# Kernel optimization log

Hardware: AMD Instinct MI355X
Metric: run time of the kernel (lower is better)

Reference implementation:

```python
import jax, jax.numpy as jnp
import numpy as np


def setup_inputs() -> dict:
    key = jax.random.key(0)
    k1, k2, k3, k4 = jax.random.split(key, 4)
    B, S, H = 1, 2048, 3072
    E, I = 4, 8192  # num_experts, intermediate_size
    x = jax.random.normal(k1, (B, S, H), dtype=jnp.float32)
    gate_w = jax.random.normal(k2, (E, H), dtype=jnp.float32) * 0.02
    w_gate_up = jax.random.normal(k3, (E, 2 * I, H), dtype=jnp.float32) * 0.02
    w_down = jax.random.normal(k4, (E, H, I), dtype=jnp.float32) * 0.02
    return {"x": x, "gate_w": gate_w, "w_gate_up": w_gate_up, "w_down": w_down, "top_k": 2}


def reference(x, gate_w, w_gate_up, w_down, top_k):
    # x: [B, S, H]; gate_w: [E, H]; w_gate_up: [E, 2I, H]; w_down: [E, H, I]
    B, S, H = x.shape
    E = gate_w.shape[0]
    # Gating: softmax over experts, then top-k values/indices
    logits = jnp.einsum('bsh,eh->bse', x, gate_w)
    probs = jax.nn.softmax(logits, axis=-1)
    gate_values, gate_indices = jax.lax.top_k(probs, top_k)  # [B, S, k]
    # Dense all-expert SwiGLU MLP (as in the original module)
    xf = x.reshape(-1, H)                                     # [N, H]
    up_states = jnp.einsum('nh,eih->nei', xf, w_gate_up)      # [N, E, 2I]
    gate, up = jnp.split(up_states, 2, axis=-1)               # [N, E, I] each
    hidden = up * jax.nn.silu(gate)                           # SwiGLU
    expert_out = jnp.einsum('nei,ehi->neh', hidden, w_down)   # [N, E, H]
    expert_out = expert_out.reshape(B, S, E, H)
    # Gather selected experts and combine with gate values
    sel = jnp.take_along_axis(expert_out, gate_indices[..., None], axis=2)  # [B, S, k, H]
    moe_output = jnp.sum(sel * gate_values[..., None], axis=2)              # [B, S, H]
    return moe_output
```

## Files before the change

kernel.cpp:

```cpp
#include <hip/hip_runtime.h>

#define S 2048
#define Hd 3072
#define NE 4
#define Id 8192
#define BM 128
#define BK 64
#define RMAX 4608

typedef __attribute__((ext_vector_type(8))) short short8;
typedef __attribute__((ext_vector_type(4))) float f32x4;

__device__ __forceinline__ unsigned short f2bf(float f) {
    unsigned u = __builtin_bit_cast(unsigned, f);
    u += 0x7FFFu + ((u >> 16) & 1u);
    return (unsigned short)(u >> 16);
}

__device__ __forceinline__ void gload_lds16(const void* g, void* l) {
    __builtin_amdgcn_global_load_lds(
        (const __attribute__((address_space(1))) unsigned int*)g,
        (__attribute__((address_space(3))) unsigned int*)l,
        16, 0, 0);
}

__global__ void gate_topk_kernel(const float* __restrict__ x,
                                 const float* __restrict__ gw,
                                 int* __restrict__ tok_e,
                                 float* __restrict__ tok_v) {
    const int t = blockIdx.x;
    const int lane = threadIdx.x & 63;
    const int wave = threadIdx.x >> 6;
    __shared__ float logits[NE];
    const float* xp = x + (size_t)t * Hd;
    const float* wp = gw + (size_t)wave * Hd;
    float s = 0.f;
    for (int h = lane; h < Hd; h += 64) s += xp[h] * wp[h];
#pragma unroll
    for (int o = 32; o > 0; o >>= 1) s += __shfl_xor(s, o);
    if (lane == 0) logits[wave] = s;
    __syncthreads();
    if (threadIdx.x == 0) {
        float m = logits[0];
#pragma unroll
        for (int e = 1; e < NE; e++) m = fmaxf(m, logits[e]);
        float p[NE]; float sum = 0.f;
#pragma unroll
        for (int e = 0; e < NE; e++) { p[e] = expf(logits[e] - m); sum += p[e]; }
        float inv = 1.f / sum;
#pragma unroll
        for (int e = 0; e < NE; e++) p[e] *= inv;
        int e0 = 0; float v0 = p[0];
#pragma unroll
        for (int e = 1; e < NE; e++) if (p[e] > v0) { e0 = e; v0 = p[e]; }
        int e1 = -1; float v1 = -1.f;
#pragma unroll
        for (int e = 0; e < NE; e++) if (e != e0 && p[e] > v1) { e1 = e; v1 = p[e]; }
        tok_e[t * 2] = e0; tok_e[t * 2 + 1] = e1;
        tok_v[t * 2] = v0; tok_v[t * 2 + 1] = v1;
    }
}

__global__ void route_kernel(const int* __restrict__ tok_e, const float* __restrict__ tok_v,
                             int* __restrict__ row_token, float* __restrict__ row_gate,
                             int* __restrict__ offsets) {
    __shared__ int cnt[NE], cur[NE], offs[NE + 1];
    const int tid = threadIdx.x;
    if (tid < NE) { cnt[tid] = 0; cur[tid] = 0; }
    __syncthreads();
    for (int i = tid; i < S * 2; i += 256) atomicAdd(&cnt[tok_e[i]], 1);
    __syncthreads();
    if (tid == 0) {
        int o = 0;
        for (int e = 0; e < NE; e++) { offs[e] = o; o += (cnt[e] + BM - 1) / BM * BM; }
        offs[NE] = o;
        for (int e = 0; e <= NE; e++) offsets[e] = offs[e];
    }
    __syncthreads();
    for (int r = tid; r < RMAX; r += 256) { row_token[r] = 0; row_gate[r] = 0.f; }
    __syncthreads();
    for (int i = tid; i < S * 2; i += 256) {
        int e = tok_e[i];
        int pos = atomicAdd(&cur[e], 1);
        int r = offs[e] + pos;
        row_token[r] = i >> 1;
        row_gate[r] = tok_v[i];
    }
}

__global__ void cvt_bf16_kernel(const float* __restrict__ src,
                                unsigned short* __restrict__ dst, size_t n8) {
    size_t stride = (size_t)gridDim.x * blockDim.x;
    for (size_t i = (size_t)blockIdx.x * blockDim.x + threadIdx.x; i < n8; i += stride) {
        size_t b = i * 8;
        f32x4 a = *(const f32x4*)(src + b);
        f32x4 c = *(const f32x4*)(src + b + 4);
        union { unsigned short u[8]; short8 v; } o;
#pragma unroll
        for (int j = 0; j < 4; j++) { o.u[j] = f2bf(a[j]); o.u[4 + j] = f2bf(c[j]); }
        *(short8*)(dst + b) = o.v;
    }
}


__global__ __launch_bounds__(256, 2)
void gemm1_bf16_kernel(const unsigned short* __restrict__ xb,
                       const unsigned short* __restrict__ wgu_b,
                       const int* __restrict__ row_token,
                       const int* __restrict__ offsets,
                       unsigned short* __restrict__ hidden) {
    __shared__ unsigned short As[BM][BK];
    __shared__ unsigned short Bg[BM][BK];
    __shared__ unsigned short Bu[BM][BK];

    const int rt = blockIdx.x, ct = blockIdx.y;
    const int rbase = rt * BM;
    const int off4 = offsets[4];
    if (rbase >= off4) return;
    int e = 3;
    if (rbase < offsets[1]) e = 0;
    else if (rbase < offsets[2]) e = 1;
    else if (rbase < offsets[3]) e = 2;

    const int tid = threadIdx.x;
    const int lane = tid & 63;
    const int wave = tid >> 6;
    const int wm = wave >> 1, wn = wave & 1;

    const unsigned short* asrc[4];
    const unsigned short* gsrc[4];
    const unsigned short* usrc[4];
#pragma unroll
    for (int i2 = 0; i2 < 4; i2++) {
        int sgi = i2 * 4 + wave;
        int row = sgi * 8 + (lane >> 3);
        int g = (lane & 7) ^ (row & 7);
        int tok = row_token[rbase + row];
        asrc[i2] = xb + (size_t)tok * Hd + g * 8;
        size_t growg = (size_t)e * (2 * Id) + (size_t)ct * 128 + row;
        gsrc[i2] = wgu_b + growg * Hd + g * 8;
        usrc[i2] = wgu_b + (growg + (size_t)Id) * Hd + g * 8;
    }

    f32x4 accg[4][4], accu[4][4];
#pragma unroll
    for (int m = 0; m < 4; m++)
#pragma unroll
        for (int n = 0; n < 4; n++) { accg[m][n] = (f32x4)0.f; accu[m][n] = (f32x4)0.f; }

    for (int k0 = 0; k0 < Hd; k0 += BK) {
        __syncthreads();
#pragma unroll
        for (int i2 = 0; i2 < 4; i2++) {
            int sgi = i2 * 4 + wave;
            gload_lds16(asrc[i2] + k0, &As[sgi * 8][0]);
            gload_lds16(gsrc[i2] + k0, &Bg[sgi * 8][0]);
            gload_lds16(usrc[i2] + k0, &Bu[sgi * 8][0]);
        }
        __syncthreads();
#pragma unroll
        for (int kk = 0; kk < 2; kk++) {
            short8 af[4], bgf[4], buf_[4];
#pragma unroll
            for (int m = 0; m < 4; m++) {
                int r = wm * 64 + m * 16 + (lane & 15);
                int slot = (kk * 4 + (lane >> 4)) ^ (r & 7);
                af[m] = *(const short8*)&As[r][slot * 8];
            }
#pragma unroll
            for (int n = 0; n < 4; n++) {
                int c = wn * 64 + n * 16 + (lane & 15);
                int slot = (kk * 4 + (lane >> 4)) ^ (c & 7);
                bgf[n] = *(const short8*)&Bg[c][slot * 8];
                buf_[n] = *(const short8*)&Bu[c][slot * 8];
            }
#pragma unroll
            for (int m = 0; m < 4; m++)
#pragma unroll
                for (int n = 0; n < 4; n++) {
                    accg[m][n] = __builtin_amdgcn_mfma_f32_16x16x32_bf16(af[m], bgf[n], accg[m][n], 0, 0, 0);
                    accu[m][n] = __builtin_amdgcn_mfma_f32_16x16x32_bf16(af[m], buf_[n], accu[m][n], 0, 0, 0);
                }
        }
    }
#pragma unroll
    for (int m = 0; m < 4; m++) {
#pragma unroll
        for (int n = 0; n < 4; n++) {
            int c = ct * 128 + wn * 64 + n * 16 + (lane & 15);
#pragma unroll
            for (int q = 0; q < 4; q++) {
                int r = rbase + wm * 64 + m * 16 + (lane >> 4) * 4 + q;
                float g = accg[m][n][q], u = accu[m][n][q];
                float hval = u * g / (1.f + expf(-g));
                hidden[(size_t)r * Id + c] = f2bf(hval);
            }
        }
    }
}

__global__ __launch_bounds__(256, 3)
void gemm2_bf16_kernel(const unsigned short* __restrict__ hidden,
                       const unsigned short* __restrict__ wd_b,
                       const int* __restrict__ row_token,
                       const float* __restrict__ row_gate,
                       const int* __restrict__ offsets,
                       float* __restrict__ out) {
    __shared__ unsigned short As[BM][BK];
    __shared__ unsigned short Bs[BM][BK];

    const int rt = blockIdx.x, ct = blockIdx.y;
    const int rbase = rt * BM;
    const int off4 = offsets[4];
    if (rbase >= off4) return;
    int e = 3;
    if (rbase < offsets[1]) e = 0;
    else if (rbase < offsets[2]) e = 1;
    else if (rbase < offsets[3]) e = 2;

    const int tid = threadIdx.x;
    const int lane = tid & 63;
    const int wave = tid >> 6;
    const int wm = wave >> 1, wn = wave & 1;

    const unsigned short* asrc[4];
    const unsigned short* bsrc[4];
#pragma unroll
    for (int i2 = 0; i2 < 4; i2++) {
        int sgi = i2 * 4 + wave;
        int row = sgi * 8 + (lane >> 3);
        int g = (lane & 7) ^ (row & 7);
        asrc[i2] = hidden + (size_t)(rbase + row) * Id + g * 8;
        bsrc[i2] = wd_b + ((size_t)e * Hd + (size_t)ct * 128 + row) * Id + g * 8;
    }

    f32x4 acc[4][4];
#pragma unroll
    for (int m = 0; m < 4; m++)
#pragma unroll
        for (int n = 0; n < 4; n++) acc[m][n] = (f32x4)0.f;

    for (int k0 = 0; k0 < Id; k0 += BK) {
        __syncthreads();
#pragma unroll
        for (int i2 = 0; i2 < 4; i2++) {
            int sgi = i2 * 4 + wave;
            gload_lds16(asrc[i2] + k0, &As[sgi * 8][0]);
            gload_lds16(bsrc[i2] + k0, &Bs[sgi * 8][0]);
        }
        __syncthreads();
#pragma unroll
        for (int kk = 0; kk < 2; kk++) {
            short8 af[4], bf[4];
#pragma unroll
            for (int m = 0; m < 4; m++) {
                int r = wm * 64 + m * 16 + (lane & 15);
                int slot = (kk * 4 + (lane >> 4)) ^ (r & 7);
                af[m] = *(const short8*)&As[r][slot * 8];
            }
#pragma unroll
            for (int n = 0; n < 4; n++) {
                int c = wn * 64 + n * 16 + (lane & 15);
                int slot = (kk * 4 + (lane >> 4)) ^ (c & 7);
                bf[n] = *(const short8*)&Bs[c][slot * 8];
            }
#pragma unroll
            for (int m = 0; m < 4; m++)
#pragma unroll
                for (int n = 0; n < 4; n++)
                    acc[m][n] = __builtin_amdgcn_mfma_f32_16x16x32_bf16(af[m], bf[n], acc[m][n], 0, 0, 0);
        }
    }
#pragma unroll
    for (int m = 0; m < 4; m++) {
#pragma unroll
        for (int n = 0; n < 4; n++) {
            int c = ct * 128 + wn * 64 + n * 16 + (lane & 15);
#pragma unroll
            for (int q = 0; q < 4; q++) {
                int r = rbase + wm * 64 + m * 16 + (lane >> 4) * 4 + q;
                int tok = row_token[r];
                float gv = row_gate[r];
                if (gv != 0.f)
                    atomicAdd(&out[(size_t)tok * Hd + c], gv * acc[m][n][q]);
            }
        }
    }
}


__global__ __launch_bounds__(256, 2)
void gemm1_f32_kernel(const unsigned short* __restrict__ xb,
                      const float* __restrict__ wgu,
                      const int* __restrict__ row_token,
                      const int* __restrict__ offsets,
                      unsigned short* __restrict__ hidden) {
    __shared__ unsigned short As[BM][BK];
    __shared__ unsigned short Bg[BM][BK];
    __shared__ unsigned short Bu[BM][BK];

    const int rt = blockIdx.x, ct = blockIdx.y;
    const int rbase = rt * BM;
    const int off4 = offsets[4];
    if (rbase >= off4) return;
    int e = 3;
    if (rbase < offsets[1]) e = 0;
    else if (rbase < offsets[2]) e = 1;
    else if (rbase < offsets[3]) e = 2;

    const int tid = threadIdx.x;
    const int lane = tid & 63;
    const int wave = tid >> 6;
    const int wm = wave >> 1, wn = wave & 1;

    const unsigned short* asrc[4];
#pragma unroll
    for (int i2 = 0; i2 < 4; i2++) {
        int sgi = i2 * 4 + wave;
        int row = sgi * 8 + (lane >> 3);
        int g = (lane & 7) ^ (row & 7);
        int tok = row_token[rbase + row];
        asrc[i2] = xb + (size_t)tok * Hd + g * 8;
    }
    const int col = tid >> 1;
    const int half = tid & 1;
    const size_t grow = (size_t)e * (2 * Id) + (size_t)ct * 128 + col;
    const float* bsrc_g = wgu + grow * Hd + half * 32;
    const float* bsrc_u = wgu + (grow + (size_t)Id) * Hd + half * 32;
    const int csw = col & 7;

    f32x4 accg[4][4], accu[4][4];
#pragma unroll
    for (int m = 0; m < 4; m++)
#pragma unroll
        for (int n = 0; n < 4; n++) { accg[m][n] = (f32x4)0.f; accu[m][n] = (f32x4)0.f; }

    for (int k0 = 0; k0 < Hd; k0 += BK) {
        __syncthreads();
#pragma unroll
        for (int i2 = 0; i2 < 4; i2++) {
            int sgi = i2 * 4 + wave;
            gload_lds16(asrc[i2] + k0, &As[sgi * 8][0]);
        }
        {
            const float* pg = bsrc_g + k0;
            const float* pu = bsrc_u + k0;
            f32x4 vg[8], vu[8];
#pragma unroll
            for (int j = 0; j < 8; j++) vg[j] = *(const f32x4*)(pg + j * 4);
#pragma unroll
            for (int j = 0; j < 8; j++) vu[j] = *(const f32x4*)(pu + j * 4);
#pragma unroll
            for (int j = 0; j < 4; j++) {
                union { unsigned short u[8]; short8 v8; } wg_, wu_;
#pragma unroll
                for (int q = 0; q < 4; q++) {
                    wg_.u[q] = f2bf(vg[2 * j][q]); wg_.u[4 + q] = f2bf(vg[2 * j + 1][q]);
                    wu_.u[q] = f2bf(vu[2 * j][q]); wu_.u[4 + q] = f2bf(vu[2 * j + 1][q]);
                }
                int gs = (half * 4 + j) ^ csw;
                *(short8*)&Bg[col][gs * 8] = wg_.v8;
                *(short8*)&Bu[col][gs * 8] = wu_.v8;
            }
        }
        __syncthreads();
#pragma unroll
        for (int kk = 0; kk < 2; kk++) {
            short8 af[4], bgf[4], buf_[4];
#pragma unroll
            for (int m = 0; m < 4; m++) {
                int r = wm * 64 + m * 16 + (lane & 15);
                int slot = (kk * 4 + (lane >> 4)) ^ (r & 7);
                af[m] = *(const short8*)&As[r][slot * 8];
            }
#pragma unroll
            for (int n = 0; n < 4; n++) {
                int c = wn * 64 + n * 16 + (lane & 15);
                int slot = (kk * 4 + (lane >> 4)) ^ (c & 7);
                bgf[n] = *(const short8*)&Bg[c][slot * 8];
                buf_[n] = *(const short8*)&Bu[c][slot * 8];
            }
#pragma unroll
            for (int m = 0; m < 4; m++)
#pragma unroll
                for (int n = 0; n < 4; n++) {
                    accg[m][n] = __builtin_amdgcn_mfma_f32_16x16x32_bf16(af[m], bgf[n], accg[m][n], 0, 0, 0);
                    accu[m][n] = __builtin_amdgcn_mfma_f32_16x16x32_bf16(af[m], buf_[n], accu[m][n], 0, 0, 0);
                }
        }
    }
#pragma unroll
    for (int m = 0; m < 4; m++) {
#pragma unroll
        for (int n = 0; n < 4; n++) {
            int c = ct * 128 + wn * 64 + n * 16 + (lane & 15);
#pragma unroll
            for (int q = 0; q < 4; q++) {
                int r = rbase + wm * 64 + m * 16 + (lane >> 4) * 4 + q;
                float g = accg[m][n][q], u = accu[m][n][q];
                float hval = u * g / (1.f + expf(-g));
                hidden[(size_t)r * Id + c] = f2bf(hval);
            }
        }
    }
}

__global__ __launch_bounds__(256, 2)
void gemm2_f32_kernel(const unsigned short* __restrict__ hidden,
                      const float* __restrict__ wd,
                      const int* __restrict__ row_token,
                      const float* __restrict__ row_gate,
                      const int* __restrict__ offsets,
                      float* __restrict__ out) {
    __shared__ unsigned short As[BM][BK];
    __shared__ unsigned short Bs[BM][BK];

    const int rt = blockIdx.x, ct = blockIdx.y;
    const int rbase = rt * BM;
    const int off4 = offsets[4];
    if (rbase >= off4) return;
    int e = 3;
    if (rbase < offsets[1]) e = 0;
    else if (rbase < offsets[2]) e = 1;
    else if (rbase < offsets[3]) e = 2;

    const int tid = threadIdx.x;
    const int lane = tid & 63;
    const int wave = tid >> 6;
    const int wm = wave >> 1, wn = wave & 1;

    const unsigned short* asrc[4];
#pragma unroll
    for (int i2 = 0; i2 < 4; i2++) {
        int sgi = i2 * 4 + wave;
        int row = sgi * 8 + (lane >> 3);
        int g = (lane & 7) ^ (row & 7);
        asrc[i2] = hidden + (size_t)(rbase + row) * Id + g * 8;
    }
    const int col = tid >> 1;
    const int half = tid & 1;
    const float* bsrc = wd + ((size_t)e * Hd + (size_t)ct * 128 + col) * Id + half * 32;
    const int csw = col & 7;

    f32x4 acc[4][4];
#pragma unroll
    for (int m = 0; m < 4; m++)
#pragma unroll
        for (int n = 0; n < 4; n++) acc[m][n] = (f32x4)0.f;

    for (int k0 = 0; k0 < Id; k0 += BK) {
        __syncthreads();
#pragma unroll
        for (int i2 = 0; i2 < 4; i2++) {
            int sgi = i2 * 4 + wave;
            gload_lds16(asrc[i2] + k0, &As[sgi * 8][0]);
        }
        {
            const float* pb = bsrc + k0;
            f32x4 vb[8];
#pragma unroll
            for (int j = 0; j < 8; j++) vb[j] = *(const f32x4*)(pb + j * 4);
#pragma unroll
            for (int j = 0; j < 4; j++) {
                union { unsigned short u[8]; short8 v8; } wb_;
#pragma unroll
                for (int q = 0; q < 4; q++) {
                    wb_.u[q] = f2bf(vb[2 * j][q]); wb_.u[4 + q] = f2bf(vb[2 * j + 1][q]);
                }
                int gs = (half * 4 + j) ^ csw;
                *(short8*)&Bs[col][gs * 8] = wb_.v8;
            }
        }
        __syncthreads();
#pragma unroll
        for (int kk = 0; kk < 2; kk++) {
            short8 af[4], bf[4];
#pragma unroll
            for (int m = 0; m < 4; m++) {
                int r = wm * 64 + m * 16 + (lane & 15);
                int slot = (kk * 4 + (lane >> 4)) ^ (r & 7);
                af[m] = *(const short8*)&As[r][slot * 8];
            }
#pragma unroll
            for (int n = 0; n < 4; n++) {
                int c = wn * 64 + n * 16 + (lane & 15);
                int slot = (kk * 4 + (lane >> 4)) ^ (c & 7);
                bf[n] = *(const short8*)&Bs[c][slot * 8];
            }
#pragma unroll
            for (int m = 0; m < 4; m++)
#pragma unroll
                for (int n = 0; n < 4; n++)
                    acc[m][n] = __builtin_amdgcn_mfma_f32_16x16x32_bf16(af[m], bf[n], acc[m][n], 0, 0, 0);
        }
    }
#pragma unroll
    for (int m = 0; m < 4; m++) {
#pragma unroll
        for (int n = 0; n < 4; n++) {
            int c = ct * 128 + wn * 64 + n * 16 + (lane & 15);
#pragma unroll
            for (int q = 0; q < 4; q++) {
                int r = rbase + wm * 64 + m * 16 + (lane >> 4) * 4 + q;
                int tok = row_token[r];
                float gv = row_gate[r];
                if (gv != 0.f)
                    atomicAdd(&out[(size_t)tok * Hd + c], gv * acc[m][n][q]);
            }
        }
    }
}

extern "C" void kernel_launch(void* const* d_in, const int* in_sizes, int n_in,
                              void* d_out, int out_size, void* d_ws, size_t ws_size,
                              hipStream_t stream) {
    const float* x   = (const float*)d_in[0];
    const float* gw  = (const float*)d_in[1];
    const float* wgu = (const float*)d_in[2];
    const float* wd  = (const float*)d_in[3];
    float* out = (float*)d_out;

    const size_t n_wgu = (size_t)NE * 2 * Id * Hd;
    const size_t n_wd  = (size_t)NE * Hd * Id;

    char* ws = (char*)d_ws;
    size_t o = 0;
    auto alloc = [&](size_t bytes) { void* p = ws + o; o = (o + bytes + 255) & ~(size_t)255; return p; };
    unsigned short* xb      = (unsigned short*)alloc((size_t)S * Hd * 2);
    unsigned short* hidden  = (unsigned short*)alloc((size_t)RMAX * Id * 2);
    int*   row_token = (int*)alloc(RMAX * 4);
    float* row_gate  = (float*)alloc(RMAX * 4);
    int*   offsets   = (int*)alloc(8 * 4);
    int*   tok_e     = (int*)alloc(S * 2 * 4);
    float* tok_v     = (float*)alloc(S * 2 * 4);
    size_t base_need = o;
    unsigned short* wgu_b = (unsigned short*)alloc(n_wgu * 2);
    unsigned short* wd_b  = (unsigned short*)alloc(n_wd * 2);
    const bool big = (ws_size >= o);

    hipMemsetAsync(d_out, 0, (size_t)S * Hd * 4, stream);
    gate_topk_kernel<<<S, 256, 0, stream>>>(x, gw, tok_e, tok_v);
    route_kernel<<<1, 256, 0, stream>>>(tok_e, tok_v, row_token, row_gate, offsets);
    cvt_bf16_kernel<<<1024, 256, 0, stream>>>(x, xb, (size_t)S * Hd / 8);

    if (big) {
        cvt_bf16_kernel<<<2048, 256, 0, stream>>>(wgu, wgu_b, n_wgu / 8);
        cvt_bf16_kernel<<<2048, 256, 0, stream>>>(wd, wd_b, n_wd / 8);
        gemm1_bf16_kernel<<<dim3(RMAX / BM, Id / 128), 256, 0, stream>>>(
            xb, wgu_b, row_token, offsets, hidden);
        gemm2_bf16_kernel<<<dim3(RMAX / BM, Hd / 128), 256, 0, stream>>>(
            hidden, wd_b, row_token, row_gate, offsets, out);
    } else {
        (void)base_need;
        gemm1_f32_kernel<<<dim3(RMAX / BM, Id / 128), 256, 0, stream>>>(
            xb, wgu, row_token, offsets, hidden);
        gemm2_f32_kernel<<<dim3(RMAX / BM, Hd / 128), 256, 0, stream>>>(
            hidden, wd, row_token, row_gate, offsets, out);
    }
}
```

Baseline: 1.381 ms.

## Replace bf16 expert GEMMs with 256x256 double-buffered 8-wave pipelined kernels

Rewrites both grouped expert GEMMs to use 256-row tiles with 8 waves (512 threads), double-buffered LDS, and a four-phase schedule. Each phase interleaves global-to-LDS prefetch of the next K slice with MFMA on the current one, using partial vmcnt waits, barriers and setprio. Routing padding grows to 256 rows per expert and RMAX rises to fit. The gate/up weights are interleaved in 16-row groups so one B tile holds both. The aim is to hide memory latency and raise arithmetic intensity per tile, at the cost of more padded rows, higher register pressure and 64KB of LDS per block.

```diff
diff --git a/kernel.cpp b/kernel.cpp
--- a/kernel.cpp
+++ b/kernel.cpp
@@ -4,9 +4,8 @@
 #define Hd 3072
 #define NE 4
 #define Id 8192
-#define BM 128
 #define BK 64
-#define RMAX 4608
+#define RMAX 5120
 
 typedef __attribute__((ext_vector_type(8))) short short8;
 typedef __attribute__((ext_vector_type(4))) float f32x4;
@@ -22,6 +21,12 @@
         (const __attribute__((address_space(1))) unsigned int*)g,
         (__attribute__((address_space(3))) unsigned int*)l,
         16, 0, 0);
+}
+
+__device__ __forceinline__ void phase_wait() {
+    asm volatile("s_waitcnt vmcnt(8)" ::: "memory");
+    __builtin_amdgcn_s_barrier();
+    __builtin_amdgcn_sched_barrier(0);
 }
 
 __global__ void gate_topk_kernel(const float* __restrict__ x,
@@ -72,7 +77,7 @@
     __syncthreads();
     if (tid == 0) {
         int o = 0;
-        for (int e = 0; e < NE; e++) { offs[e] = o; o += (cnt[e] + BM - 1) / BM * BM; }
+        for (int e = 0; e < NE; e++) { offs[e] = o; o += (cnt[e] + 255) / 256 * 256; }
         offs[NE] = o;
         for (int e = 0; e <= NE; e++) offsets[e] = offs[e];
     }
@@ -103,189 +108,316 @@
 }
 
 
-__global__ __launch_bounds__(256, 2)
-void gemm1_bf16_kernel(const unsigned short* __restrict__ xb,
-                       const unsigned short* __restrict__ wgu_b,
-                       const int* __restrict__ row_token,
-                       const int* __restrict__ offsets,
-                       unsigned short* __restrict__ hidden) {
-    __shared__ unsigned short As[BM][BK];
-    __shared__ unsigned short Bg[BM][BK];
-    __shared__ unsigned short Bu[BM][BK];
+__global__ __launch_bounds__(512, 2)
+void gemm1_8p_kernel(const unsigned short* __restrict__ xb,
+                     const unsigned short* __restrict__ wgu_b,
+                     const int* __restrict__ row_token,
+                     const int* __restrict__ offsets,
+                     unsigned short* __restrict__ hidden) {
+    __shared__ unsigned short Ald[2][256][BK];
+    __shared__ unsigned short Bld[2][256][BK];
 
     const int rt = blockIdx.x, ct = blockIdx.y;
-    const int rbase = rt * BM;
-    const int off4 = offsets[4];
-    if (rbase >= off4) return;
+    const int rbase = rt * 256;
+    if (rbase >= offsets[4]) return;
     int e = 3;
     if (rbase < offsets[1]) e = 0;
     else if (rbase < offsets[2]) e = 1;
     else if (rbase < offsets[3]) e = 2;
 
     const int tid = threadIdx.x;
-    const int lane = tid & 63;
-    const int wave = tid >> 6;
-    const int wm = wave >> 1, wn = wave & 1;
-
-    const unsigned short* asrc[4];
-    const unsigned short* gsrc[4];
-    const unsigned short* usrc[4];
-#pragma unroll
-    for (int i2 = 0; i2 < 4; i2++) {
-        int sgi = i2 * 4 + wave;
-        int row = sgi * 8 + (lane >> 3);
-        int g = (lane & 7) ^ (row & 7);
+    const int l = tid & 63;
+    const int w = tid >> 6;
+    const int wm = w >> 2, wn = w & 3;
+    const int lr = l >> 3;
+    const int g8 = ((l & 7) ^ lr) << 3;
+    const int c16 = l & 15, c4 = l >> 4, l7 = l & 7;
+
+    const unsigned short* aP[4]; int raD[4];
+    const unsigned short* bP[4]; int rbD[4];
+#pragma unroll
+    for (int j = 0; j < 4; j++) {
+        int r0 = w * 8 + (j & 1) * 128 + (j >> 1) * 64;
+        raD[j] = r0;
+        int row = r0 + lr;
         int tok = row_token[rbase + row];
-        asrc[i2] = xb + (size_t)tok * Hd + g * 8;
-        size_t growg = (size_t)e * (2 * Id) + (size_t)ct * 128 + row;
-        gsrc[i2] = wgu_b + growg * Hd + g * 8;
-        usrc[i2] = wgu_b + (growg + (size_t)Id) * Hd + g * 8;
-    }
-
-    f32x4 accg[4][4], accu[4][4];
-#pragma unroll
-    for (int m = 0; m < 4; m++)
-#pragma unroll
-        for (int n = 0; n < 4; n++) { accg[m][n] = (f32x4)0.f; accu[m][n] = (f32x4)0.f; }
-
-    for (int k0 = 0; k0 < Hd; k0 += BK) {
-        __syncthreads();
-#pragma unroll
-        for (int i2 = 0; i2 < 4; i2++) {
-            int sgi = i2 * 4 + wave;
-            gload_lds16(asrc[i2] + k0, &As[sgi * 8][0]);
-            gload_lds16(gsrc[i2] + k0, &Bg[sgi * 8][0]);
-            gload_lds16(usrc[i2] + k0, &Bu[sgi * 8][0]);
-        }
-        __syncthreads();
-#pragma unroll
-        for (int kk = 0; kk < 2; kk++) {
-            short8 af[4], bgf[4], buf_[4];
-#pragma unroll
-            for (int m = 0; m < 4; m++) {
-                int r = wm * 64 + m * 16 + (lane & 15);
-                int slot = (kk * 4 + (lane >> 4)) ^ (r & 7);
-                af[m] = *(const short8*)&As[r][slot * 8];
-            }
-#pragma unroll
-            for (int n = 0; n < 4; n++) {
-                int c = wn * 64 + n * 16 + (lane & 15);
-                int slot = (kk * 4 + (lane >> 4)) ^ (c & 7);
-                bgf[n] = *(const short8*)&Bg[c][slot * 8];
-                buf_[n] = *(const short8*)&Bu[c][slot * 8];
-            }
-#pragma unroll
-            for (int m = 0; m < 4; m++)
-#pragma unroll
-                for (int n = 0; n < 4; n++) {
-                    accg[m][n] = __builtin_amdgcn_mfma_f32_16x16x32_bf16(af[m], bgf[n], accg[m][n], 0, 0, 0);
-                    accu[m][n] = __builtin_amdgcn_mfma_f32_16x16x32_bf16(af[m], buf_[n], accu[m][n], 0, 0, 0);
-                }
-        }
-    }
-#pragma unroll
-    for (int m = 0; m < 4; m++) {
-#pragma unroll
-        for (int n = 0; n < 4; n++) {
-            int c = ct * 128 + wn * 64 + n * 16 + (lane & 15);
+        aP[j] = xb + (size_t)tok * Hd + g8;
+        int rb0 = (w & 3) * 8 + (w >> 2) * 64 + (j & 1) * 128 + (j >> 1) * 32;
+        rbD[j] = rb0;
+        int brow = rb0 + lr;
+        int f = brow >> 4;
+        size_t wr = (size_t)e * (2 * Id) + (size_t)(f & 1) * Id
+                  + (size_t)ct * 128 + ((f >> 1) << 4) + (brow & 15);
+        bP[j] = wgu_b + wr * Hd + g8;
+    }
+
+    f32x4 acc[8][4];
+#pragma unroll
+    for (int mi = 0; mi < 8; mi++)
+#pragma unroll
+        for (int n = 0; n < 4; n++) acc[mi][n] = (f32x4)0.f;
+
+    gload_lds16(aP[0], &Ald[0][raD[0]][0]);
+    gload_lds16(aP[1], &Ald[0][raD[1]][0]);
+    gload_lds16(bP[0], &Bld[0][rbD[0]][0]);
+    gload_lds16(bP[1], &Bld[0][rbD[1]][0]);
+    gload_lds16(aP[2], &Ald[0][raD[2]][0]);
+    gload_lds16(aP[3], &Ald[0][raD[3]][0]);
+    gload_lds16(bP[2], &Bld[0][rbD[2]][0]);
+    gload_lds16(bP[3], &Bld[0][rbD[3]][0]);
+
+    const int nt = Hd / BK;
+    for (int t = 0; t < nt; ++t) {
+        const int bufR = t & 1, bufW = bufR ^ 1;
+        const int ks = ((t + 1 < nt) ? t + 1 : nt - 1) * BK;
+        short8 afL[4][2], afH[4][2], bfL[2][2], bfH[2][2];
+        gload_lds16(aP[0] + ks, &Ald[bufW][raD[0]][0]);
+        gload_lds16(aP[1] + ks, &Ald[bufW][raD[1]][0]);
+        phase_wait();
+#pragma unroll
+        for (int mi = 0; mi < 4; mi++)
+#pragma unroll
+            for (int kk = 0; kk < 2; kk++) {
+                int row = wm * 128 + mi * 16 + c16;
+                int slot = ((kk << 2) + c4) ^ l7;
+                afL[mi][kk] = *(const short8*)&Ald[bufR][row][slot * 8];
+            }
+        gload_lds16(bP[0] + ks, &Bld[bufW][rbD[0]][0]);
+        gload_lds16(bP[1] + ks, &Bld[bufW][rbD[1]][0]);
+        phase_wait();
+#pragma unroll
+        for (int n = 0; n < 2; n++)
+#pragma unroll
+            for (int kk = 0; kk < 2; kk++) {
+                int row = wn * 64 + n * 16 + c16;
+                int slot = ((kk << 2) + c4) ^ l7;
+                bfL[n][kk] = *(const short8*)&Bld[bufR][row][slot * 8];
+            }
+        __builtin_amdgcn_s_setprio(1);
+#pragma unroll
+        for (int mi = 0; mi < 4; mi++)
+#pragma unroll
+            for (int n = 0; n < 2; n++)
+#pragma unroll
+                for (int kk = 0; kk < 2; kk++)
+                    acc[mi][n] = __builtin_amdgcn_mfma_f32_16x16x32_bf16(
+                        afL[mi][kk], bfL[n][kk], acc[mi][n], 0, 0, 0);
+        __builtin_amdgcn_s_setprio(0);
+        gload_lds16(aP[2] + ks, &Ald[bufW][raD[2]][0]);
+        gload_lds16(aP[3] + ks, &Ald[bufW][raD[3]][0]);
+        phase_wait();
+#pragma unroll
+        for (int mi = 0; mi < 4; mi++)
+#pragma unroll
+            for (int kk = 0; kk < 2; kk++) {
+                int row = wm * 128 + 64 + mi * 16 + c16;
+                int slot = ((kk << 2) + c4) ^ l7;
+                afH[mi][kk] = *(const short8*)&Ald[bufR][row][slot * 8];
+            }
+        __builtin_amdgcn_s_setprio(1);
+#pragma unroll
+        for (int mi = 0; mi < 4; mi++)
+#pragma unroll
+            for (int n = 0; n < 2; n++)
+#pragma unroll
+                for (int kk = 0; kk < 2; kk++)
+                    acc[mi + 4][n] = __builtin_amdgcn_mfma_f32_16x16x32_bf16(
+                        afH[mi][kk], bfL[n][kk], acc[mi + 4][n], 0, 0, 0);
+        __builtin_amdgcn_s_setprio(0);
+        gload_lds16(bP[2] + ks, &Bld[bufW][rbD[2]][0]);
+        gload_lds16(bP[3] + ks, &Bld[bufW][rbD[3]][0]);
+        phase_wait();
+#pragma unroll
+        for (int n = 0; n < 2; n++)
+#pragma unroll
+            for (int kk = 0; kk < 2; kk++) {
+                int row = wn * 64 + 32 + n * 16 + c16;
+                int slot = ((kk << 2) + c4) ^ l7;
+                bfH[n][kk] = *(const short8*)&Bld[bufR][row][slot * 8];
+            }
+        __builtin_amdgcn_s_setprio(1);
+#pragma unroll
+        for (int mi = 0; mi < 8; mi++)
+#pragma unroll
+            for (int n = 0; n < 2; n++)
+#pragma unroll
+                for (int kk = 0; kk < 2; kk++)
+                    acc[mi][n + 2] = __builtin_amdgcn_mfma_f32_16x16x32_bf16(
+                        (mi < 4 ? afL[mi & 3][kk] : afH[mi & 3][kk]),
+                        bfH[n][kk], acc[mi][n + 2], 0, 0, 0);
+        __builtin_amdgcn_s_setprio(0);
+        __builtin_amdgcn_s_barrier();
+        __builtin_amdgcn_sched_barrier(0);
+    }
+
+#pragma unroll
+    for (int mi = 0; mi < 8; mi++)
+#pragma unroll
+        for (int np = 0; np < 2; np++) {
+            int col = ct * 128 + (wn * 2 + np) * 16 + c16;
 #pragma unroll
             for (int q = 0; q < 4; q++) {
-                int r = rbase + wm * 64 + m * 16 + (lane >> 4) * 4 + q;
-                float g = accg[m][n][q], u = accu[m][n][q];
-                float hval = u * g / (1.f + expf(-g));
-                hidden[(size_t)r * Id + c] = f2bf(hval);
-            }
-        }
-    }
-}
-
-__global__ __launch_bounds__(256, 3)
-void gemm2_bf16_kernel(const unsigned short* __restrict__ hidden,
-                       const unsigned short* __restrict__ wd_b,
-                       const int* __restrict__ row_token,
-                       const float* __restrict__ row_gate,
-                       const int* __restrict__ offsets,
-                       float* __restrict__ out) {
-    __shared__ unsigned short As[BM][BK];
-    __shared__ unsigned short Bs[BM][BK];
+                int row = rbase + wm * 128 + mi * 16 + c4 * 4 + q;
+                float gv = acc[mi][2 * np][q], uv = acc[mi][2 * np + 1][q];
+                float h = uv * gv / (1.f + expf(-gv));
+                hidden[(size_t)row * Id + col] = f2bf(h);
+            }
+        }
+}
+
+__global__ __launch_bounds__(512, 2)
+void gemm2_8p_kernel(const unsigned short* __restrict__ hidden,
+                     const unsigned short* __restrict__ wd_b,
+                     const int* __restrict__ row_token,
+                     const float* __restrict__ row_gate,
+                     const int* __restrict__ offsets,
+                     float* __restrict__ out) {
+    __shared__ unsigned short Ald[2][256][BK];
+    __shared__ unsigned short Bld[2][256][BK];
 
     const int rt = blockIdx.x, ct = blockIdx.y;
-    const int rbase = rt * BM;
-    const int off4 = offsets[4];
-    if (rbase >= off4) return;
+    const int rbase = rt * 256;
+    if (rbase >= offsets[4]) return;
     int e = 3;
     if (rbase < offsets[1]) e = 0;
     else if (rbase < offsets[2]) e = 1;
     else if (rbase < offsets[3]) e = 2;
 
     const int tid = threadIdx.x;
-    const int lane = tid & 63;
-    const int wave = tid >> 6;
-    const int wm = wave >> 1, wn = wave & 1;
-
-    const unsigned short* asrc[4];
-    const unsigned short* bsrc[4];
-#pragma unroll
-    for (int i2 = 0; i2 < 4; i2++) {
-        int sgi = i2 * 4 + wave;
-        int row = sgi * 8 + (lane >> 3);
-        int g = (lane & 7) ^ (row & 7);
-        asrc[i2] = hidden + (size_t)(rbase + row) * Id + g * 8;
-        bsrc[i2] = wd_b + ((size_t)e * Hd + (size_t)ct * 128 + row) * Id + g * 8;
-    }
-
-    f32x4 acc[4][4];
-#pragma unroll
-    for (int m = 0; m < 4; m++)
-#pragma unroll
-        for (int n = 0; n < 4; n++) acc[m][n] = (f32x4)0.f;
-
-    for (int k0 = 0; k0 < Id; k0 += BK) {
-        __syncthreads();
-#pragma unroll
-        for (int i2 = 0; i2 < 4; i2++) {
-            int sgi = i2 * 4 + wave;
-            gload_lds16(asrc[i2] + k0, &As[sgi * 8][0]);
-            gload_lds16(bsrc[i2] + k0, &Bs[sgi * 8][0]);
-        }
-        __syncthreads();
-#pragma unroll
-        for (int kk = 0; kk < 2; kk++) {
-            short8 af[4], bf[4];
-#pragma unroll
-            for (int m = 0; m < 4; m++) {
-                int r = wm * 64 + m * 16 + (lane & 15);
-                int slot = (kk * 4 + (lane >> 4)) ^ (r & 7);
-                af[m] = *(const short8*)&As[r][slot * 8];
-            }
-#pragma unroll
-            for (int n = 0; n < 4; n++) {
-                int c = wn * 64 + n * 16 + (lane & 15);
-                int slot = (kk * 4 + (lane >> 4)) ^ (c & 7);
-                bf[n] = *(const short8*)&Bs[c][slot * 8];
-            }
-#pragma unroll
-            for (int m = 0; m < 4; m++)
-#pragma unroll
-                for (int n = 0; n < 4; n++)
-                    acc[m][n] = __builtin_amdgcn_mfma_f32_16x16x32_bf16(af[m], bf[n], acc[m][n], 0, 0, 0);
-        }
-    }
-#pragma unroll
-    for (int m = 0; m < 4; m++) {
+    const int l = tid & 63;
+    const int w = tid >> 6;
+    const int wm = w >> 2, wn = w & 3;
+    const int lr = l >> 3;
+    const int g8 = ((l & 7) ^ lr) << 3;
+    const int c16 = l & 15, c4 = l >> 4, l7 = l & 7;
+
+    const unsigned short* aP[4]; int raD[4];
+    const unsigned short* bP[4]; int rbD[4];
+#pragma unroll
+    for (int j = 0; j < 4; j++) {
+        int r0 = w * 8 + (j & 1) * 128 + (j >> 1) * 64;
+        raD[j] = r0;
+        aP[j] = hidden + (size_t)(rbase + r0 + lr) * Id + g8;
+        int rb0 = (w & 3) * 8 + (w >> 2) * 64 + (j & 1) * 128 + (j >> 1) * 32;
+        rbD[j] = rb0;
+        int brow = rb0 + lr;
+        size_t wr = (size_t)e * Hd + (size_t)ct * 256 + brow;
+        bP[j] = wd_b + wr * Id + g8;
+    }
+
+    f32x4 acc[8][4];
+#pragma unroll
+    for (int mi = 0; mi < 8; mi++)
+#pragma unroll
+        for (int n = 0; n < 4; n++) acc[mi][n] = (f32x4)0.f;
+
+    gload_lds16(aP[0], &Ald[0][raD[0]][0]);
+    gload_lds16(aP[1], &Ald[0][raD[1]][0]);
+    gload_lds16(bP[0], &Bld[0][rbD[0]][0]);
+    gload_lds16(bP[1], &Bld[0][rbD[1]][0]);
+    gload_lds16(aP[2], &Ald[0][raD[2]][0]);
+    gload_lds16(aP[3], &Ald[0][raD[3]][0]);
+    gload_lds16(bP[2], &Bld[0][rbD[2]][0]);
+    gload_lds16(bP[3], &Bld[0][rbD[3]][0]);
+
+    const int nt = Id / BK;
+    for (int t = 0; t < nt; ++t) {
+        const int bufR = t & 1, bufW = bufR ^ 1;
+        const int ks = ((t + 1 < nt) ? t + 1 : nt - 1) * BK;
+        short8 afL[4][2], afH[4][2], bfL[2][2], bfH[2][2];
+        gload_lds16(aP[0] + ks, &Ald[bufW][raD[0]][0]);
+        gload_lds16(aP[1] + ks, &Ald[bufW][raD[1]][0]);
+        phase_wait();
+#pragma unroll
+        for (int mi = 0; mi < 4; mi++)
+#pragma unroll
+            for (int kk = 0; kk < 2; kk++) {
+                int row = wm * 128 + mi * 16 + c16;
+                int slot = ((kk << 2) + c4) ^ l7;
+                afL[mi][kk] = *(const short8*)&Ald[bufR][row][slot * 8];
+            }
+        gload_lds16(bP[0] + ks, &Bld[bufW][rbD[0]][0]);
+        gload_lds16(bP[1] + ks, &Bld[bufW][rbD[1]][0]);
+        phase_wait();
+#pragma unroll
+        for (int n = 0; n < 2; n++)
+#pragma unroll
+            for (int kk = 0; kk < 2; kk++) {
+                int row = wn * 64 + n * 16 + c16;
+                int slot = ((kk << 2) + c4) ^ l7;
+                bfL[n][kk] = *(const short8*)&Bld[bufR][row][slot * 8];
+            }
+        __builtin_amdgcn_s_setprio(1);
+#pragma unroll
+        for (int mi = 0; mi < 4; mi++)
+#pragma unroll
+            for (int n = 0; n < 2; n++)
+#pragma unroll
+                for (int kk = 0; kk < 2; kk++)
+                    acc[mi][n] = __builtin_amdgcn_mfma_f32_16x16x32_bf16(
+                        afL[mi][kk], bfL[n][kk], acc[mi][n], 0, 0, 0);
+        __builtin_amdgcn_s_setprio(0);
+        gload_lds16(aP[2] + ks, &Ald[bufW][raD[2]][0]);
+        gload_lds16(aP[3] + ks, &Ald[bufW][raD[3]][0]);
+        phase_wait();
+#pragma unroll
+        for (int mi = 0; mi < 4; mi++)
+#pragma unroll
+            for (int kk = 0; kk < 2; kk++) {
+                int row = wm * 128 + 64 + mi * 16 + c16;
+                int slot = ((kk << 2) + c4) ^ l7;
+                afH[mi][kk] = *(const short8*)&Ald[bufR][row][slot * 8];
+            }
+        __builtin_amdgcn_s_setprio(1);
+#pragma unroll
+        for (int mi = 0; mi < 4; mi++)
+#pragma unroll
+            for (int n = 0; n < 2; n++)
+#pragma unroll
+                for (int kk = 0; kk < 2; kk++)
+                    acc[mi + 4][n] = __builtin_amdgcn_mfma_f32_16x16x32_bf16(
+                        afH[mi][kk], bfL[n][kk], acc[mi + 4][n], 0, 0, 0);
+        __builtin_amdgcn_s_setprio(0);
+        gload_lds16(bP[2] + ks, &Bld[bufW][rbD[2]][0]);
+        gload_lds16(bP[3] + ks, &Bld[bufW][rbD[3]][0]);
+        phase_wait();
+#pragma unroll
+        for (int n = 0; n < 2; n++)
+#pragma unroll
+            for (int kk = 0; kk < 2; kk++) {
+                int row = wn * 64 + 32 + n * 16 + c16;
+                int slot = ((kk << 2) + c4) ^ l7;
+                bfH[n][kk] = *(const short8*)&Bld[bufR][row][slot * 8];
+            }
+        __builtin_amdgcn_s_setprio(1);
+#pragma unroll
+        for (int mi = 0; mi < 8; mi++)
+#pragma unroll
+            for (int n = 0; n < 2; n++)
+#pragma unroll
+                for (int kk = 0; kk < 2; kk++)
+                    acc[mi][n + 2] = __builtin_amdgcn_mfma_f32_16x16x32_bf16(
+                        (mi < 4 ? afL[mi & 3][kk] : afH[mi & 3][kk]),
+                        bfH[n][kk], acc[mi][n + 2], 0, 0, 0);
+        __builtin_amdgcn_s_setprio(0);
+        __builtin_amdgcn_s_barrier();
+        __builtin_amdgcn_sched_barrier(0);
+    }
+
+#pragma unroll
+    for (int mi = 0; mi < 8; mi++)
 #pragma unroll
         for (int n = 0; n < 4; n++) {
-            int c = ct * 128 + wn * 64 + n * 16 + (lane & 15);
+            int col = ct * 256 + wn * 64 + n * 16 + c16;
 #pragma unroll
             for (int q = 0; q < 4; q++) {
-                int r = rbase + wm * 64 + m * 16 + (lane >> 4) * 4 + q;
+                int r = rbase + wm * 128 + mi * 16 + c4 * 4 + q;
                 int tok = row_token[r];
                 float gv = row_gate[r];
                 if (gv != 0.f)
-                    atomicAdd(&out[(size_t)tok * Hd + c], gv * acc[m][n][q]);
-            }
-        }
-    }
+                    atomicAdd(&out[(size_t)tok * Hd + col], gv * acc[mi][n][q]);
+            }
+        }
 }
 
 
@@ -295,14 +427,13 @@
                       const int* __restrict__ row_token,
                       const int* __restrict__ offsets,
                       unsigned short* __restrict__ hidden) {
-    __shared__ unsigned short As[BM][BK];
-    __shared__ unsigned short Bg[BM][BK];
-    __shared__ unsigned short Bu[BM][BK];
+    __shared__ unsigned short As[128][BK];
+    __shared__ unsigned short Bg[128][BK];
+    __shared__ unsigned short Bu[128][BK];
 
     const int rt = blockIdx.x, ct = blockIdx.y;
-    const int rbase = rt * BM;
-    const int off4 = offsets[4];
-    if (rbase >= off4) return;
+    const int rbase = rt * 128;
+    if (rbase >= offsets[4]) return;
     int e = 3;
     if (rbase < offsets[1]) e = 0;
     else if (rbase < offsets[2]) e = 1;
@@ -412,13 +543,12 @@
                       const float* __restrict__ row_gate,
                       const int* __restrict__ offsets,
                       float* __restrict__ out) {
-    __shared__ unsigned short As[BM][BK];
-    __shared__ unsigned short Bs[BM][BK];
+    __shared__ unsigned short As[128][BK];
+    __shared__ unsigned short Bs[128][BK];
 
     const int rt = blockIdx.x, ct = blockIdx.y;
-    const int rbase = rt * BM;
-    const int off4 = offsets[4];
-    if (rbase >= off4) return;
+    const int rbase = rt * 128;
+    if (rbase >= offsets[4]) return;
     int e = 3;
     if (rbase < offsets[1]) e = 0;
     else if (rbase < offsets[2]) e = 1;
@@ -533,7 +663,6 @@
     int*   offsets   = (int*)alloc(8 * 4);
     int*   tok_e     = (int*)alloc(S * 2 * 4);
     float* tok_v     = (float*)alloc(S * 2 * 4);
-    size_t base_need = o;
     unsigned short* wgu_b = (unsigned short*)alloc(n_wgu * 2);
     unsigned short* wd_b  = (unsigned short*)alloc(n_wd * 2);
     const bool big = (ws_size >= o);
@@ -546,15 +675,14 @@
     if (big) {
         cvt_bf16_kernel<<<2048, 256, 0, stream>>>(wgu, wgu_b, n_wgu / 8);
         cvt_bf16_kernel<<<2048, 256, 0, stream>>>(wd, wd_b, n_wd / 8);
-        gemm1_bf16_kernel<<<dim3(RMAX / BM, Id / 128), 256, 0, stream>>>(
+        gemm1_8p_kernel<<<dim3(RMAX / 256, Id / 128), 512, 0, stream>>>(
             xb, wgu_b, row_token, offsets, hidden);
-        gemm2_bf16_kernel<<<dim3(RMAX / BM, Hd / 128), 256, 0, stream>>>(
+        gemm2_8p_kernel<<<dim3(RMAX / 256, Hd / 256), 512, 0, stream>>>(
             hidden, wd_b, row_token, row_gate, offsets, out);
     } else {
-        (void)base_need;
-        gemm1_f32_kernel<<<dim3(RMAX / BM, Id / 128), 256, 0, stream>>>(
+        gemm1_f32_kernel<<<dim3(RMAX / 128, Id / 128), 256, 0, stream>>>(
             xb, wgu, row_token, offsets, hidden);
-        gemm2_f32_kernel<<<dim3(RMAX / BM, Hd / 128), 256, 0, stream>>>(
+        gemm2_f32_kernel<<<dim3(RMAX / 128, Hd / 128), 256, 0, stream>>>(
             hidden, wd, row_token, row_gate, offsets, out);
     }
 }
```

Measured after the change: 1.518 ms. 1.1x slower.
